# Performance work log

Hardware: AMD Instinct MI355X
Metric: run time of the kernel (lower is better)

## Reference

```python
import jax, jax.numpy as jnp
import numpy as np

WS = 14          # window size
NH = 12          # num heads
C = 768          # hidden dim
HD = C // NH     # head dim = 64
MLP = 3072       # mlp dim
EPS = 1e-6


def _layernorm(x, g, b):
    mu = jnp.mean(x, axis=-1, keepdims=True)
    var = jnp.mean(jnp.square(x - mu), axis=-1, keepdims=True)
    return (x - mu) * jax.lax.rsqrt(var + EPS) * g + b


def setup_inputs() -> dict:
    key = jax.random.key(0)
    ks = jax.random.split(key, 8)
    B, H, W = 8, 64, 64
    f32 = jnp.float32
    d = {}
    d["x"] = jax.random.normal(ks[0], (B, H, W, C), f32)
    d["ln1_g"] = jnp.ones((C,), f32)
    d["ln1_b"] = jnp.zeros((C,), f32)
    d["qkv_w"] = (jax.random.normal(ks[1], (C, 3 * C), f32) * 0.02)
    d["qkv_b"] = jnp.zeros((3 * C,), f32)
    d["proj_w"] = (jax.random.normal(ks[2], (C, C), f32) * 0.02)
    d["proj_b"] = jnp.zeros((C,), f32)
    d["rel_pos_h"] = (jax.random.normal(ks[3], (2 * WS - 1, HD), f32) * 0.02)
    d["rel_pos_w"] = (jax.random.normal(ks[4], (2 * WS - 1, HD), f32) * 0.02)
    d["ln2_g"] = jnp.ones((C,), f32)
    d["ln2_b"] = jnp.zeros((C,), f32)
    d["mlp_w1"] = (jax.random.normal(ks[5], (C, MLP), f32) * 0.02)
    d["mlp_b1"] = jnp.zeros((MLP,), f32)
    d["mlp_w2"] = (jax.random.normal(ks[6], (MLP, C), f32) * 0.02)
    d["mlp_b2"] = jnp.zeros((C,), f32)
    return d


def reference(x, ln1_g, ln1_b, qkv_w, qkv_b, proj_w, proj_b,
              rel_pos_h, rel_pos_w, ln2_g, ln2_b,
              mlp_w1, mlp_b1, mlp_w2, mlp_b2):
    B, H, W, _ = x.shape
    xn = _layernorm(x, ln1_g, ln1_b)

    # ---- window partition (pad to multiple of WS) ----
    pad_h = (-H) % WS
    pad_w = (-W) % WS
    Hp, Wp = H + pad_h, W + pad_w
    xp = jnp.pad(xn, ((0, 0), (0, pad_h), (0, pad_w), (0, 0)))
    # [B, Hp/WS, WS, Wp/WS, WS, C] -> [Bn, WS, WS, C]
    win = xp.reshape(B, Hp // WS, WS, Wp // WS, WS, C)
    win = win.transpose(0, 1, 3, 2, 4, 5).reshape(-1, WS, WS, C)
    Bn = win.shape[0]
    N = WS * WS

    # ---- attention with decomposed relative position bias ----
    qkv = win.reshape(Bn, N, C) @ qkv_w + qkv_b                 # [Bn, N, 3C]
    qkv = qkv.reshape(Bn, N, 3, NH, HD).transpose(2, 0, 3, 1, 4)
    qkv = qkv.reshape(3, Bn * NH, N, HD)
    q, k, v = qkv[0], qkv[1], qkv[2]

    scale = HD ** -0.5
    attn = jnp.einsum('bnd,bmd->bnm', q * scale, k)             # [Bn*NH, N, N]

    # rel coords: q_size == k_size == WS, rel_pos already has 2*WS-1 rows
    coords = jnp.arange(WS)[:, None] - jnp.arange(WS)[None, :] + (WS - 1)
    Rh = rel_pos_h[coords]                                      # [WS, WS, HD]
    Rw = rel_pos_w[coords]                                      # [WS, WS, HD]
    rq = q.reshape(Bn * NH, WS, WS, HD)
    rel_h = jnp.einsum('bhwc,hkc->bhwk', rq, Rh)                # [B', WS, WS, WS]
    rel_w = jnp.einsum('bhwc,wkc->bhwk', rq, Rw)
    attn = (attn.reshape(Bn * NH, WS, WS, WS, WS)
            + rel_h[:, :, :, :, None]
            + rel_w[:, :, :, None, :]).reshape(Bn * NH, N, N)

    attn = jax.nn.softmax(attn, axis=-1)
    out = jnp.einsum('bnm,bmd->bnd', attn, v)                   # [Bn*NH, N, HD]
    out = out.reshape(Bn, NH, WS, WS, HD).transpose(0, 2, 3, 1, 4).reshape(Bn, WS, WS, C)
    out = out @ proj_w + proj_b

    # ---- window unpartition ----
    out = out.reshape(B, Hp // WS, Wp // WS, WS, WS, C)
    out = out.transpose(0, 1, 3, 2, 4, 5).reshape(B, Hp, Wp, C)[:, :H, :W, :]

    x1 = x + out
    y = _layernorm(x1, ln2_g, ln2_b)
    y = jax.nn.gelu(y @ mlp_w1 + mlp_b1, approximate=False) @ mlp_w2 + mlp_b2
    return x1 + y
```

## Files before the change

kernel.cpp:

```cpp
#include <hip/hip_runtime.h>
#include <hip/hip_bf16.h>
#include <cstdint>
#include <cstddef>

using bf16 = __hip_bfloat16;
typedef __attribute__((ext_vector_type(8))) short short8;
typedef __attribute__((ext_vector_type(4))) float f32x4;

typedef __attribute__((address_space(1))) const void as1_void;
typedef __attribute__((address_space(3))) void as3_void;

__device__ __forceinline__ f32x4 mfma16x16x32(short8 a, short8 b, f32x4 c) {
  return __builtin_amdgcn_mfma_f32_16x16x32_bf16(a, b, c, 0, 0, 0);
}

__device__ __forceinline__ void gload_lds16(const void* g, void* l) {
  __builtin_amdgcn_global_load_lds((as1_void*)g, (as3_void*)l, 16, 0, 0);
}

__device__ __forceinline__ uint32_t cvtpk(float a, float b) {
  uint32_t r;
  asm("v_cvt_pk_bf16_f32 %0, %1, %2" : "=v"(r) : "v"(a), "v"(b));
  return r;
}

__device__ __forceinline__ float gelu_f(float v) {
  const float u = 0.7978845608f * v * (1.f + 0.044715f * v * v);
  const float e = __expf(-2.f * fabsf(u));
  const float t = (1.f - e) / (1.f + e);
  return 0.5f * v * (1.f + (u < 0.f ? -t : t));
}

static constexpr int MROWS = 39200;
static constexpr int MPAD  = 39296;
static constexpr int TOK2  = 32768;

__global__ __launch_bounds__(256)
void transpose_cast(const float* __restrict__ in, bf16* __restrict__ out, int K, int N) {
  __shared__ float t[32][33];
  const int tx = threadIdx.x & 31, ty = threadIdx.x >> 5;
  const int bx = blockIdx.x, by = blockIdx.y;
  const int x = bx * 32 + tx;
  for (int r = ty; r < 32; r += 8)
    t[r][tx] = in[(size_t)(by * 32 + r) * N + x];
  __syncthreads();
  const int xo = by * 32 + tx;
  for (int r = ty; r < 32; r += 8)
    out[(size_t)(bx * 32 + r) * K + xo] = __float2bfloat16(t[tx][r]);
}

__global__ __launch_bounds__(256)
void ln1_partition(const float* __restrict__ x, const float* __restrict__ g,
                   const float* __restrict__ bb, bf16* __restrict__ out) {
  const int token = blockIdx.x * 4 + (threadIdx.x >> 6);
  const int lane = threadIdx.x & 63;
  const int win = token / 196, tok = token % 196;
  const int b_ = win / 25, wh = (win / 5) % 5, ww = win % 5;
  const int i = tok / 14, j = tok % 14;
  const int h = wh * 14 + i, w = ww * 14 + j;
  bf16* o = out + (size_t)token * 768;
  if (h >= 64 || w >= 64) {
    for (int t = 0; t < 12; ++t) o[lane + 64 * t] = __float2bfloat16(0.f);
    return;
  }
  const float* src = x + ((size_t)((b_ * 64 + h) * 64 + w)) * 768;
  float vals[12], s = 0.f, ss = 0.f;
  #pragma unroll
  for (int t = 0; t < 12; ++t) {
    float v = src[lane + 64 * t];
    vals[t] = v; s += v; ss += v * v;
  }
  #pragma unroll
  for (int d = 32; d > 0; d >>= 1) { s += __shfl_xor(s, d); ss += __shfl_xor(ss, d); }
  const float mu = s * (1.f / 768.f);
  const float var = ss * (1.f / 768.f) - mu * mu;
  const float inv = rsqrtf(var + 1e-6f);
  #pragma unroll
  for (int t = 0; t < 12; ++t) {
    const int c = lane + 64 * t;
    o[c] = __float2bfloat16((vals[t] - mu) * inv * g[c] + bb[c]);
  }
}

__global__ __launch_bounds__(256)
void ln2_kernel(const float* __restrict__ x1, const float* __restrict__ g,
                const float* __restrict__ bb, bf16* __restrict__ out) {
  const int token = blockIdx.x * 4 + (threadIdx.x >> 6);
  const int lane = threadIdx.x & 63;
  const float* src = x1 + (size_t)token * 768;
  bf16* o = out + (size_t)token * 768;
  float vals[12], s = 0.f, ss = 0.f;
  #pragma unroll
  for (int t = 0; t < 12; ++t) {
    float v = src[lane + 64 * t];
    vals[t] = v; s += v; ss += v * v;
  }
  #pragma unroll
  for (int d = 32; d > 0; d >>= 1) { s += __shfl_xor(s, d); ss += __shfl_xor(ss, d); }
  const float mu = s * (1.f / 768.f);
  const float var = ss * (1.f / 768.f) - mu * mu;
  const float inv = rsqrtf(var + 1e-6f);
  #pragma unroll
  for (int t = 0; t < 12; ++t) {
    const int c = lane + 64 * t;
    o[c] = __float2bfloat16((vals[t] - mu) * inv * g[c] + bb[c]);
  }
}

template<int EPI>
__global__ __launch_bounds__(256)
void gemm_bf16(const bf16* __restrict__ A, const bf16* __restrict__ Bt,
               const float* __restrict__ bias, int K, int Mreal,
               const float* __restrict__ fin, float* __restrict__ fout,
               bf16* __restrict__ ob0, bf16* __restrict__ ob1, bf16* __restrict__ ob2) {
  __shared__ __align__(16) bf16 SMEM[16384];
  bf16* const lA0 = SMEM;
  bf16* const lA1 = SMEM + 4096;
  bf16* const lB0 = SMEM + 8192;
  bf16* const lB1 = SMEM + 12288;
  const int tid = threadIdx.x;
  const int lane = tid & 63, wv = tid >> 6;
  const int lr = lane & 15, hi = lane >> 4;
  const int wm = wv >> 1, wn = wv & 1;

  const int gx = gridDim.x;
  const int nwg = gx * gridDim.y;
  int lin = blockIdx.y * gx + blockIdx.x;
  {
    const int q8 = nwg >> 3, r8 = nwg & 7;
    const int xcd = lin & 7, pos = lin >> 3;
    lin = (xcd < r8 ? xcd * (q8 + 1) : r8 * (q8 + 1) + (xcd - r8) * q8) + pos;
  }
  const size_t arow0 = (size_t)(lin / gx) * 128;
  const size_t brow0 = (size_t)(lin % gx) * 128;
  f32x4 acc[4][4] = {};

  auto stage = [&](bf16* bufA, bf16* bufB, int kt) {
    const int k0 = kt * 32;
    #pragma unroll
    for (int it = 0; it < 2; ++it) {
      const int seg = it * 256 + tid;
      const int row = seg >> 2, kq = seg & 3;
      const size_t dst = (size_t)(it * 256 + wv * 64) * 8;
      if constexpr (EPI == 1) {
        const int k = k0 + kq * 8;
        gload_lds16(A + ((size_t)(k >> 6) * MPAD + arow0 + row) * 64 + (k & 63), bufA + dst);
      } else {
        gload_lds16(A + (arow0 + row) * K + k0 + kq * 8, bufA + dst);
      }
      gload_lds16(Bt + (brow0 + row) * K + k0 + kq * 8, bufB + dst);
    }
  };
  auto compute = [&](const bf16* bufA, const bf16* bufB) {
    short8 af[4], bfr[4];
    #pragma unroll
    for (int m = 0; m < 4; ++m) af[m] = *(const short8*)&bufA[(wm * 64 + m * 16 + lr) * 32 + hi * 8];
    #pragma unroll
    for (int n = 0; n < 4; ++n) bfr[n] = *(const short8*)&bufB[(wn * 64 + n * 16 + lr) * 32 + hi * 8];
    #pragma unroll
    for (int m = 0; m < 4; ++m)
      #pragma unroll
      for (int n = 0; n < 4; ++n)
        acc[m][n] = mfma16x16x32(af[m], bfr[n], acc[m][n]);
  };

  const int nt = K >> 5;
  stage(lA0, lB0, 0);
  __syncthreads();
  for (int t = 0; t < nt; t += 2) {
    if (t + 1 < nt) stage(lA1, lB1, t + 1);
    compute(lA0, lB0);
    __syncthreads();
    if (t + 2 < nt) stage(lA0, lB0, t + 2);
    compute(lA1, lB1);
    __syncthreads();
  }

  if constexpr (EPI == 0) {
    bf16* ct = SMEM;
    #pragma unroll
    for (int n = 0; n < 4; ++n) {
      const int col = wn * 64 + n * 16 + lr;
      const float bv = bias[(int)brow0 + col];
      #pragma unroll
      for (int m = 0; m < 4; ++m) {
        #pragma unroll
        for (int e = 0; e < 4; ++e) {
          const int row = wm * 64 + m * 16 + hi * 4 + e;
          const float v = acc[m][n][e] + bv;
          const int byte = (row << 8) + (col << 1);
          *(bf16*)((char*)ct + (byte ^ ((row & 7) << 5))) = __float2bfloat16(v);
        }
      }
    }
    __syncthreads();
    #pragma unroll
    for (int i = 0; i < 8; ++i) {
      const int lin16 = i * 256 + tid;
      const int row = lin16 >> 4;
      const int u   = lin16 & 15;
      const int byte = (row << 8) + (u << 4);
      const short8 val = *(const short8*)((char*)ct + (byte ^ ((row & 7) << 5)));
      const int grow = (int)arow0 + row;
      const int gcol = (int)brow0 + u * 8;
      if (grow < Mreal) {
        const int which = gcol / 768, head = (gcol >> 6) % 12, d = gcol & 63;
        bf16* dstb = (which == 0) ? ob0 : ((which == 1) ? ob1 : ob2);
        *(short8*)&dstb[((size_t)head * MPAD + grow) * 64 + d] = val;
      }
    }
  } else {
    #pragma unroll
    for (int n = 0; n < 4; ++n) {
      const int col = (int)brow0 + wn * 64 + n * 16 + lr;
      const float bv = bias[col];
      #pragma unroll
      for (int m = 0; m < 4; ++m) {
        #pragma unroll
        for (int e = 0; e < 4; ++e) {
          const int row = (int)arow0 + wm * 64 + m * 16 + hi * 4 + e;
          const float v = acc[m][n][e] + bv;
          if (row < Mreal) {
            const int win = row / 196, tok = row % 196;
            const int b_ = win / 25, wh = (win / 5) % 5, ww = win % 5;
            const int i = tok / 14, j = tok % 14;
            const int h = wh * 14 + i, w = ww * 14 + j;
            if (h < 64 && w < 64) {
              const size_t idx = ((size_t)((b_ * 64 + h) * 64 + w)) * 768 + col;
              fout[idx] = fin[idx] + v;
            }
          }
        }
      }
    }
  }
}

template<int EPI>
__global__ __launch_bounds__(512)
void gemm256(const bf16* __restrict__ A, const bf16* __restrict__ Bt,
             const float* __restrict__ bias, int K,
             const float* __restrict__ fin, float* __restrict__ fout,
             bf16* __restrict__ ob0) {
  __shared__ __align__(16) char SMEM[65536];
  char* const bA0 = SMEM;
  char* const bB0 = SMEM + 16384;
  char* const bA1 = SMEM + 32768;
  char* const bB1 = SMEM + 49152;
  const int tid = threadIdx.x;
  const int lane = tid & 63, wv = tid >> 6;
  const int lr = lane & 15, hi = lane >> 4;
  const int wm = wv >> 2, wn = wv & 3;

  const int gx = gridDim.x;
  const int nwg = gx * gridDim.y;
  int lin = blockIdx.y * gx + blockIdx.x;
  {
    const int q8 = nwg >> 3, r8 = nwg & 7;
    const int xcd = lin & 7, pos = lin >> 3;
    lin = (xcd < r8 ? xcd * (q8 + 1) : r8 * (q8 + 1) + (xcd - r8) * q8) + pos;
  }
  const size_t arow0 = (size_t)(lin / gx) * 256;
  const size_t brow0 = (size_t)(lin % gx) * 256;

  f32x4 acc[8][4] = {};

  auto stage = [&](int kt, char* dA, char* dB) {
    const int k0 = kt * 32;
    #pragma unroll
    for (int j = 0; j < 2; ++j) {
      const int unit = j * 512 + tid;
      const int r = unit >> 2, s = unit & 3;
      const int kk = ((s ^ (r & 3)) << 3);
      gload_lds16(A + (arow0 + r) * (size_t)K + k0 + kk, dA + unit * 16);
      gload_lds16(Bt + (brow0 + r) * (size_t)K + k0 + kk, dB + unit * 16);
    }
  };
  auto compute = [&](const char* sA, const char* sB) {
    short8 bfr[4];
    #pragma unroll
    for (int n = 0; n < 4; ++n) {
      const int br = wn * 64 + n * 16 + lr;
      bfr[n] = *(const short8*)(sB + br * 64 + ((hi ^ (br & 3)) << 4));
    }
    #pragma unroll
    for (int m = 0; m < 8; ++m) {
      const int ar = wm * 128 + m * 16 + lr;
      const short8 af = *(const short8*)(sA + ar * 64 + ((hi ^ (ar & 3)) << 4));
      #pragma unroll
      for (int n = 0; n < 4; ++n)
        acc[m][n] = mfma16x16x32(af, bfr[n], acc[m][n]);
    }
  };

  const int nt = K >> 5;
  stage(0, bA0, bB0);
  stage(1, bA1, bB1);
  for (int t = 0; t < nt; t += 2) {
    asm volatile("s_waitcnt vmcnt(4)" ::: "memory");
    __builtin_amdgcn_s_barrier();
    __builtin_amdgcn_s_setprio(1);
    compute(bA0, bB0);
    __builtin_amdgcn_s_setprio(0);
    asm volatile("s_waitcnt lgkmcnt(0)" ::: "memory");
    __builtin_amdgcn_s_barrier();
    if (t + 2 < nt) { stage(t + 2, bA0, bB0);
                      asm volatile("s_waitcnt vmcnt(4)" ::: "memory"); }
    else            { asm volatile("s_waitcnt vmcnt(0)" ::: "memory"); }
    __builtin_amdgcn_s_barrier();
    __builtin_amdgcn_s_setprio(1);
    compute(bA1, bB1);
    __builtin_amdgcn_s_setprio(0);
    asm volatile("s_waitcnt lgkmcnt(0)" ::: "memory");
    __builtin_amdgcn_s_barrier();
    if (t + 3 < nt) stage(t + 3, bA1, bB1);
  }

  if constexpr (EPI == 2) {
    char* ep = SMEM + wv * 8192;
    #pragma unroll
    for (int h = 0; h < 2; ++h) {
      #pragma unroll
      for (int m2 = 0; m2 < 4; ++m2) {
        #pragma unroll
        for (int n = 0; n < 4; ++n) {
          const int col = n * 16 + lr;
          const float bv = bias[(int)brow0 + wn * 64 + col];
          #pragma unroll
          for (int e = 0; e < 4; ++e) {
            const int row_l = m2 * 16 + hi * 4 + e;
            const float v = gelu_f(acc[h * 4 + m2][n][e] + bv);
            *(bf16*)(ep + row_l * 128 + (((col >> 3) ^ (row_l & 7)) << 4) + ((col & 7) << 1))
                = __float2bfloat16(v);
          }
        }
      }
      #pragma unroll
      for (int p = 0; p < 8; ++p) {
        const int row_l = p * 8 + (lane >> 3);
        const int slot  = lane & 7;
        const short8 val = *(const short8*)(ep + row_l * 128 + ((slot ^ (row_l & 7)) << 4));
        const size_t grow = arow0 + wm * 128 + h * 64 + row_l;
        const int gcol = (int)brow0 + wn * 64 + slot * 8;
        *(short8*)&ob0[grow * 3072 + gcol] = val;
      }
    }
  } else {
    #pragma unroll
    for (int n = 0; n < 4; ++n) {
      const int col = (int)brow0 + wn * 64 + n * 16 + lr;
      const float bv = bias[col];
      #pragma unroll
      for (int m = 0; m < 8; ++m) {
        #pragma unroll
        for (int e = 0; e < 4; ++e) {
          const size_t row = arow0 + wm * 128 + m * 16 + hi * 4 + e;
          const size_t idx = row * 768 + col;
          fout[idx] = fin[idx] + acc[m][n][e] + bv;
        }
      }
    }
  }
}

__global__ __launch_bounds__(512, 2)
void attn_kernel(const bf16* __restrict__ qb, const bf16* __restrict__ kb,
                 const bf16* __restrict__ vb, const float* __restrict__ rph,
                 const float* __restrict__ rpw, bf16* __restrict__ aout) {
  __shared__ __align__(16) char SM[65248];
  bf16* pbh    = (bf16*)SM;
  bf16* pbw    = (bf16*)(SM + 4096);
  bf16* Gh     = (bf16*)(SM + 8192);
  bf16* Gw     = (bf16*)(SM + 23168);
  char* klds   = SM;
  char* vtb    = SM + 25600;
  bf16* relh_s = (bf16*)(SM + 54272);
  bf16* relw_s = (bf16*)(SM + 59760);

  const int bh = blockIdx.x;
  const int win = bh / 12, head = bh % 12;
  const size_t base = ((size_t)head * MPAD + win * 196) * 64;
  const bf16* Q  = qb + base;
  const bf16* Kp = kb + base;
  const bf16* Vp = vb + base;
  const int tid = threadIdx.x, lane = tid & 63, wv = tid >> 6;
  const int lr = lane & 15, hi = lane >> 4;

  for (int i = tid; i < 32 * 64; i += 512) {
    const int r = i >> 6, c = i & 63;
    const bool ok = r < 27;
    pbh[i] = __float2bfloat16(ok ? rph[r * 64 + c] : 0.f);
    pbw[i] = __float2bfloat16(ok ? rpw[r * 64 + c] : 0.f);
  }
  __syncthreads();
  {
    short8 bh00 = *(const short8*)&pbh[(lr) * 64 + hi * 8];
    short8 bh01 = *(const short8*)&pbh[(lr) * 64 + 32 + hi * 8];
    short8 bh10 = *(const short8*)&pbh[(16 + lr) * 64 + hi * 8];
    short8 bh11 = *(const short8*)&pbh[(16 + lr) * 64 + 32 + hi * 8];
    short8 bw00 = *(const short8*)&pbw[(lr) * 64 + hi * 8];
    short8 bw01 = *(const short8*)&pbw[(lr) * 64 + 32 + hi * 8];
    short8 bw10 = *(const short8*)&pbw[(16 + lr) * 64 + hi * 8];
    short8 bw11 = *(const short8*)&pbw[(16 + lr) * 64 + 32 + hi * 8];
    for (int mt = wv; mt < 13; mt += 8) {
      const short8 a0 = *(const short8*)&Q[(mt * 16 + lr) * 64 + hi * 8];
      const short8 a1 = *(const short8*)&Q[(mt * 16 + lr) * 64 + 32 + hi * 8];
      f32x4 g0 = {}, g1 = {}, g2 = {}, g3 = {};
      g0 = mfma16x16x32(a0, bh00, g0); g0 = mfma16x16x32(a1, bh01, g0);
      g1 = mfma16x16x32(a0, bh10, g1); g1 = mfma16x16x32(a1, bh11, g1);
      g2 = mfma16x16x32(a0, bw00, g2); g2 = mfma16x16x32(a1, bw01, g2);
      g3 = mfma16x16x32(a0, bw10, g3); g3 = mfma16x16x32(a1, bw11, g3);
      #pragma unroll
      for (int e = 0; e < 4; ++e) {
        const int row = mt * 16 + hi * 4 + e;
        Gh[row * 36 + lr]      = __float2bfloat16(g0[e]);
        Gh[row * 36 + 16 + lr] = __float2bfloat16(g1[e]);
        Gw[row * 36 + lr]      = __float2bfloat16(g2[e]);
        Gw[row * 36 + 16 + lr] = __float2bfloat16(g3[e]);
      }
    }
  }
  __syncthreads();
  bf16 ghr[6], gwr[6];
  #pragma unroll
  for (int t = 0; t < 6; ++t) {
    const int i = tid + t * 512;
    if (i < 196 * 14) {
      const int q = i / 14, kk = i - (i / 14) * 14;
      const int rh = q / 14 - kk + 13;
      const int rw2 = q - (q / 14) * 14 - kk + 13;
      ghr[t] = Gh[q * 36 + rh];
      gwr[t] = Gw[q * 36 + rw2];
    }
  }
  __syncthreads();
  #pragma unroll
  for (int t = 0; t < 6; ++t) {
    const int i = tid + t * 512;
    if (i < 196 * 14) { relh_s[i] = ghr[t]; relw_s[i] = gwr[t]; }
  }
  for (int c = wv; c < 25; c += 8) {
    const int row = c * 8 + (lane >> 3);
    const int ch  = (lane & 7) ^ (row & 7);
    gload_lds16(Kp + row * 64 + ch * 8, klds + c * 1024);
  }
  for (int i = tid; i < 196 * 8; i += 512) {
    const int key = i >> 3, dg = (i & 7) * 8;
    const short8 v = *(const short8*)&Vp[key * 64 + dg];
    #pragma unroll
    for (int j = 0; j < 8; ++j) {
      const int idx = (dg + j) * 448 + key * 2;
      *(bf16*)(vtb + (idx ^ (j << 4))) = ((const bf16*)&v)[j];
    }
  }
  for (int i = tid; i < 64 * 28; i += 512) {
    const int d = i / 28, key = 196 + i - (i / 28) * 28;
    const int idx = d * 448 + key * 2;
    *(bf16*)(vtb + (idx ^ ((d & 7) << 4))) = __float2bfloat16(0.f);
  }
  __syncthreads();

  for (int qt = wv; qt < 13; qt += 8) {
    const int q = qt * 16 + lr;
    const int qc = q < 196 ? q : 195;
    const short8 bq0 = *(const short8*)&Q[(qt * 16 + lr) * 64 + hi * 8];
    const short8 bq1 = *(const short8*)&Q[(qt * 16 + lr) * 64 + 32 + hi * 8];
    f32x4 s[13];
    __builtin_amdgcn_s_setprio(1);
    #pragma unroll
    for (int nt = 0; nt < 13; ++nt) {
      const int key = nt * 16 + lr;
      const char* kr = klds + key * 128;
      const short8 ka0 = *(const short8*)(kr + (((hi) ^ (key & 7)) << 4));
      const short8 ka1 = *(const short8*)(kr + (((hi + 4) ^ (key & 7)) << 4));
      f32x4 z = {};
      z = mfma16x16x32(ka0, bq0, z);
      z = mfma16x16x32(ka1, bq1, z);
      s[nt] = z;
    }
    __builtin_amdgcn_s_setprio(0);
    float mx = -3.0e38f;
    #pragma unroll
    for (int nt = 0; nt < 13; ++nt) {
      #pragma unroll
      for (int e = 0; e < 4; ++e) {
        const int key = nt * 16 + hi * 4 + e;
        const int kh = key / 14, kw = key - kh * 14;
        float v = s[nt][e] * 0.125f + __bfloat162float(relh_s[qc * 14 + kh])
                                    + __bfloat162float(relw_s[qc * 14 + kw]);
        v = (key < 196) ? v : -3.0e38f;
        s[nt][e] = v;
        mx = fmaxf(mx, v);
      }
    }
    mx = fmaxf(mx, __shfl_xor(mx, 16));
    mx = fmaxf(mx, __shfl_xor(mx, 32));
    float sm = 0.f;
    uint32_t pk0[14], pk1[14];
    #pragma unroll
    for (int nt = 0; nt < 13; ++nt) {
      const float p0 = __expf(s[nt][0] - mx);
      const float p1 = __expf(s[nt][1] - mx);
      const float p2 = __expf(s[nt][2] - mx);
      const float p3 = __expf(s[nt][3] - mx);
      sm += (p0 + p1) + (p2 + p3);
      pk0[nt] = cvtpk(p0, p1);
      pk1[nt] = cvtpk(p2, p3);
    }
    pk0[13] = 0u; pk1[13] = 0u;
    sm += __shfl_xor(sm, 16);
    sm += __shfl_xor(sm, 32);
    const float rinv = 1.f / sm;
    f32x4 o[4] = {};
    #pragma unroll
    for (int kk = 0; kk < 7; ++kk) {
      const uint32_t x0 = pk0[2 * kk],     x1 = pk1[2 * kk];
      const uint32_t y0 = pk0[2 * kk + 1], y1 = pk1[2 * kk + 1];
      const uint32_t s0 = (hi < 2) ? y0 : x0, s1 = (hi < 2) ? y1 : x1;
      const uint32_t t0 = __shfl_xor(s0, 32), t1 = __shfl_xor(s1, 32);
      const uint32_t o0 = (hi < 2) ? x0 : y0, o1 = (hi < 2) ? x1 : y1;
      const bool sendOwn = (hi == 1) || (hi == 2);
      const uint32_t u0 = sendOwn ? o0 : t0, u1 = sendOwn ? o1 : t1;
      const uint32_t r0 = __shfl_xor(u0, 16), r1 = __shfl_xor(u1, 16);
      union { uint32_t u[4]; short8 v; } pf;
      pf.u[0] = (hi == 0) ? x0 : ((hi == 2) ? t0 : r0);
      pf.u[1] = (hi == 0) ? x1 : ((hi == 2) ? t1 : r1);
      pf.u[2] = (hi == 3) ? y0 : ((hi == 1) ? t0 : r0);
      pf.u[3] = (hi == 3) ? y1 : ((hi == 1) ? t1 : r1);
      __builtin_amdgcn_s_setprio(1);
      #pragma unroll
      for (int n2 = 0; n2 < 4; ++n2) {
        const int d = n2 * 16 + lr;
        const int idx = d * 448 + (kk * 32 + hi * 8) * 2;
        const short8 va = *(const short8*)(vtb + (idx ^ ((lr & 7) << 4)));
        o[n2] = mfma16x16x32(va, pf.v, o[n2]);
      }
      __builtin_amdgcn_s_setprio(0);
    }
    if (q < 196) {
      bf16* orow = aout + ((size_t)head * MPAD + win * 196 + q) * 64;
      #pragma unroll
      for (int n2 = 0; n2 < 4; ++n2) {
        uint32_t d0 = cvtpk(o[n2][0] * rinv, o[n2][1] * rinv);
        uint32_t d1 = cvtpk(o[n2][2] * rinv, o[n2][3] * rinv);
        uint32_t* dst = (uint32_t*)&orow[n2 * 16 + hi * 4];
        dst[0] = d0; dst[1] = d1;
      }
    }
  }
}

extern "C" void kernel_launch(void* const* d_in, const int* in_sizes, int n_in,
                              void* d_out, int out_size, void* d_ws, size_t ws_size,
                              hipStream_t stream) {
  (void)in_sizes; (void)n_in; (void)out_size; (void)ws_size;
  const float* x      = (const float*)d_in[0];
  const float* ln1_g  = (const float*)d_in[1];
  const float* ln1_b  = (const float*)d_in[2];
  const float* qkv_w  = (const float*)d_in[3];
  const float* qkv_b  = (const float*)d_in[4];
  const float* proj_w = (const float*)d_in[5];
  const float* proj_b = (const float*)d_in[6];
  const float* rph    = (const float*)d_in[7];
  const float* rpw    = (const float*)d_in[8];
  const float* ln2_g  = (const float*)d_in[9];
  const float* ln2_b  = (const float*)d_in[10];
  const float* w1     = (const float*)d_in[11];
  const float* b1v    = (const float*)d_in[12];
  const float* w2     = (const float*)d_in[13];
  const float* b2v    = (const float*)d_in[14];
  float* outp = (float*)d_out;

  char* ws = (char*)d_ws;
  size_t off = 0;
  auto alloc = [&](size_t bytes) { char* p = ws + off; off += (bytes + 255) & ~(size_t)255; return p; };
  bf16* qkv_wt  = (bf16*)alloc((size_t)2304 * 768 * 2);
  bf16* proj_wt = (bf16*)alloc((size_t)768 * 768 * 2);
  bf16* w1t     = (bf16*)alloc((size_t)3072 * 768 * 2);
  bf16* w2t     = (bf16*)alloc((size_t)768 * 3072 * 2);
  const size_t szB1 = (size_t)MPAD * 768 * 2;
  const size_t szB2 = (size_t)TOK2 * 768 * 2;
  char* regB = alloc(szB1 > szB2 ? szB1 : szB2);
  const size_t szQKV = (size_t)3 * 12 * MPAD * 64 * 2;
  const size_t szH   = (size_t)TOK2 * 3072 * 2;
  char* regC = alloc(szQKV > szH ? szQKV : szH);

  bf16* xnwin   = (bf16*)regB;
  bf16* attnout = (bf16*)regB;
  bf16* xn2     = (bf16*)regB;
  bf16* qbuf    = (bf16*)regC;
  bf16* kbuf    = qbuf + (size_t)12 * MPAD * 64;
  bf16* vbuf    = kbuf + (size_t)12 * MPAD * 64;
  bf16* hbuf    = (bf16*)regC;

  transpose_cast<<<dim3(2304 / 32, 768 / 32), 256, 0, stream>>>(qkv_w, qkv_wt, 768, 2304);
  transpose_cast<<<dim3(768 / 32, 768 / 32), 256, 0, stream>>>(proj_w, proj_wt, 768, 768);
  transpose_cast<<<dim3(3072 / 32, 768 / 32), 256, 0, stream>>>(w1, w1t, 768, 3072);
  transpose_cast<<<dim3(768 / 32, 3072 / 32), 256, 0, stream>>>(w2, w2t, 3072, 768);

  ln1_partition<<<dim3(MROWS / 4), 256, 0, stream>>>(x, ln1_g, ln1_b, xnwin);

  gemm_bf16<0><<<dim3(2304 / 128, MPAD / 128), 256, 0, stream>>>(
      xnwin, qkv_wt, qkv_b, 768, MROWS, nullptr, nullptr, qbuf, kbuf, vbuf);

  attn_kernel<<<dim3(2400), 512, 0, stream>>>(qbuf, kbuf, vbuf, rph, rpw, attnout);

  gemm_bf16<1><<<dim3(768 / 128, MPAD / 128), 256, 0, stream>>>(
      attnout, proj_wt, proj_b, 768, MROWS, x, outp, nullptr, nullptr, nullptr);

  ln2_kernel<<<dim3(TOK2 / 4), 256, 0, stream>>>(outp, ln2_g, ln2_b, xn2);

  gemm256<2><<<dim3(3072 / 256, TOK2 / 256), 512, 0, stream>>>(
      xn2, w1t, b1v, 768, nullptr, nullptr, hbuf);
  gemm256<3><<<dim3(768 / 256, TOK2 / 256), 512, 0, stream>>>(
      hbuf, w2t, b2v, 3072, outp, outp, nullptr);
}
```

Measured before the change: 1.113 ms.

## Restructure 256x256 GEMM main loop with BK=64 tiles and staggered A/B prefetch

Doubles the K-tile from 32 to 64, which doubles the LDS footprint to 128 KiB, and switches to a new XOR swizzle over 8 16-byte slots. The loop is rewritten as an explicitly unrolled tile routine. A and B loads for future tiles are issued at different points inside the MFMA sequence, so global-to-LDS traffic overlaps compute and there are fewer barriers per K step. The risks are the higher LDS use, which allows only one workgroup per CU, more register pressure, and a subtle wait-count and buffer-reuse protocol that is easy to get wrong.

```diff
diff --git a/kernel.cpp b/kernel.cpp
--- a/kernel.cpp
+++ b/kernel.cpp
@@ -242,11 +242,11 @@
              const float* __restrict__ bias, int K,
              const float* __restrict__ fin, float* __restrict__ fout,
              bf16* __restrict__ ob0) {
-  __shared__ __align__(16) char SMEM[65536];
-  char* const bA0 = SMEM;
-  char* const bB0 = SMEM + 16384;
-  char* const bA1 = SMEM + 32768;
-  char* const bB1 = SMEM + 49152;
+  __shared__ __align__(16) char SMEM[131072];
+  char* const A0 = SMEM;
+  char* const B0 = SMEM + 32768;
+  char* const A1 = SMEM + 65536;
+  char* const B1 = SMEM + 98304;
   const int tid = threadIdx.x;
   const int lane = tid & 63, wv = tid >> 6;
   const int lr = lane & 15, hi = lane >> 4;
@@ -264,59 +264,94 @@
   const size_t brow0 = (size_t)(lin % gx) * 256;
 
   f32x4 acc[8][4] = {};
-
-  auto stage = [&](int kt, char* dA, char* dB) {
-    const int k0 = kt * 32;
-    #pragma unroll
-    for (int j = 0; j < 2; ++j) {
-      const int unit = j * 512 + tid;
-      const int r = unit >> 2, s = unit & 3;
-      const int kk = ((s ^ (r & 3)) << 3);
-      gload_lds16(A + (arow0 + r) * (size_t)K + k0 + kk, dA + unit * 16);
-      gload_lds16(Bt + (brow0 + r) * (size_t)K + k0 + kk, dB + unit * 16);
+  const int nt = K >> 6;
+
+  auto stageOp = [&](int kt, char* dst, const bf16* src, size_t row0) {
+    const int k0 = kt << 6;
+    const int rr = tid >> 3, sd = tid & 7;
+    #pragma unroll
+    for (int s = 0; s < 4; ++s) {
+      const int r = s * 64 + rr;
+      const int q = sd ^ ((r >> 1) & 7);
+      gload_lds16(src + (row0 + r) * (size_t)K + k0 + q * 8, dst + s * 8192 + (tid << 4));
     }
   };
-  auto compute = [&](const char* sA, const char* sB) {
-    short8 bfr[4];
-    #pragma unroll
-    for (int n = 0; n < 4; ++n) {
-      const int br = wn * 64 + n * 16 + lr;
-      bfr[n] = *(const short8*)(sB + br * 64 + ((hi ^ (br & 3)) << 4));
-    }
-    #pragma unroll
-    for (int m = 0; m < 8; ++m) {
-      const int ar = wm * 128 + m * 16 + lr;
-      const short8 af = *(const short8*)(sA + ar * 64 + ((hi ^ (ar & 3)) << 4));
-      #pragma unroll
-      for (int n = 0; n < 4; ++n)
-        acc[m][n] = mfma16x16x32(af, bfr[n], acc[m][n]);
-    }
+  auto rdA = [&](const char* buf, int mt, int kk) -> short8 {
+    const int r = wm * 128 + mt * 16 + lr;
+    const int slot = (kk * 4 + hi) ^ ((r >> 1) & 7);
+    return *(const short8*)(buf + r * 128 + (slot << 4));
   };
-
-  const int nt = K >> 5;
-  stage(0, bA0, bB0);
-  stage(1, bA1, bB1);
+  auto rdB = [&](const char* buf, int n, int kk) -> short8 {
+    const int r = wn * 64 + n * 16 + lr;
+    const int slot = (kk * 4 + hi) ^ ((r >> 1) & 7);
+    return *(const short8*)(buf + r * 128 + (slot << 4));
+  };
+
+  auto tile = [&](int t, char* cA, char* cB, char* oA) {
+    if (t + 1 >= nt) asm volatile("s_waitcnt vmcnt(0)" ::: "memory");
+    else             asm volatile("s_waitcnt vmcnt(4)" ::: "memory");
+    __builtin_amdgcn_s_barrier();
+    if (t + 1 < nt) stageOp(t + 1, oA, A, arow0);
+    short8 a0 = rdA(cA, 0, 0), a1 = rdA(cA, 1, 0), a2 = rdA(cA, 2, 0), a3 = rdA(cA, 3, 0);
+    short8 b0 = rdB(cB, 0, 0), b1 = rdB(cB, 1, 0), b2 = rdB(cB, 2, 0), b3 = rdB(cB, 3, 0);
+    __builtin_amdgcn_s_setprio(1);
+    acc[0][0] = mfma16x16x32(a0, b0, acc[0][0]); acc[0][1] = mfma16x16x32(a0, b1, acc[0][1]);
+    acc[0][2] = mfma16x16x32(a0, b2, acc[0][2]); acc[0][3] = mfma16x16x32(a0, b3, acc[0][3]);
+    acc[1][0] = mfma16x16x32(a1, b0, acc[1][0]); acc[1][1] = mfma16x16x32(a1, b1, acc[1][1]);
+    acc[1][2] = mfma16x16x32(a1, b2, acc[1][2]); acc[1][3] = mfma16x16x32(a1, b3, acc[1][3]);
+    acc[2][0] = mfma16x16x32(a2, b0, acc[2][0]); acc[2][1] = mfma16x16x32(a2, b1, acc[2][1]);
+    acc[2][2] = mfma16x16x32(a2, b2, acc[2][2]); acc[2][3] = mfma16x16x32(a2, b3, acc[2][3]);
+    acc[3][0] = mfma16x16x32(a3, b0, acc[3][0]); acc[3][1] = mfma16x16x32(a3, b1, acc[3][1]);
+    acc[3][2] = mfma16x16x32(a3, b2, acc[3][2]); acc[3][3] = mfma16x16x32(a3, b3, acc[3][3]);
+    __builtin_amdgcn_s_setprio(0);
+    short8 a4 = rdA(cA, 4, 0), a5 = rdA(cA, 5, 0), a6 = rdA(cA, 6, 0), a7 = rdA(cA, 7, 0);
+    __builtin_amdgcn_s_setprio(1);
+    acc[4][0] = mfma16x16x32(a4, b0, acc[4][0]); acc[4][1] = mfma16x16x32(a4, b1, acc[4][1]);
+    acc[4][2] = mfma16x16x32(a4, b2, acc[4][2]); acc[4][3] = mfma16x16x32(a4, b3, acc[4][3]);
+    acc[5][0] = mfma16x16x32(a5, b0, acc[5][0]); acc[5][1] = mfma16x16x32(a5, b1, acc[5][1]);
+    acc[5][2] = mfma16x16x32(a5, b2, acc[5][2]); acc[5][3] = mfma16x16x32(a5, b3, acc[5][3]);
+    acc[6][0] = mfma16x16x32(a6, b0, acc[6][0]); acc[6][1] = mfma16x16x32(a6, b1, acc[6][1]);
+    acc[6][2] = mfma16x16x32(a6, b2, acc[6][2]); acc[6][3] = mfma16x16x32(a6, b3, acc[6][3]);
+    acc[7][0] = mfma16x16x32(a7, b0, acc[7][0]); acc[7][1] = mfma16x16x32(a7, b1, acc[7][1]);
+    acc[7][2] = mfma16x16x32(a7, b2, acc[7][2]); acc[7][3] = mfma16x16x32(a7, b3, acc[7][3]);
+    __builtin_amdgcn_s_setprio(0);
+    a0 = rdA(cA, 0, 1); a1 = rdA(cA, 1, 1); a2 = rdA(cA, 2, 1); a3 = rdA(cA, 3, 1);
+    b0 = rdB(cB, 0, 1); b1 = rdB(cB, 1, 1); b2 = rdB(cB, 2, 1); b3 = rdB(cB, 3, 1);
+    __builtin_amdgcn_s_setprio(1);
+    acc[0][0] = mfma16x16x32(a0, b0, acc[0][0]); acc[0][1] = mfma16x16x32(a0, b1, acc[0][1]);
+    acc[0][2] = mfma16x16x32(a0, b2, acc[0][2]); acc[0][3] = mfma16x16x32(a0, b3, acc[0][3]);
+    acc[1][0] = mfma16x16x32(a1, b0, acc[1][0]); acc[1][1] = mfma16x16x32(a1, b1, acc[1][1]);
+    acc[1][2] = mfma16x16x32(a1, b2, acc[1][2]); acc[1][3] = mfma16x16x32(a1, b3, acc[1][3]);
+    acc[2][0] = mfma16x16x32(a2, b0, acc[2][0]); acc[2][1] = mfma16x16x32(a2, b1, acc[2][1]);
+    acc[2][2] = mfma16x16x32(a2, b2, acc[2][2]); acc[2][3] = mfma16x16x32(a2, b3, acc[2][3]);
+    acc[3][0] = mfma16x16x32(a3, b0, acc[3][0]); acc[3][1] = mfma16x16x32(a3, b1, acc[3][1]);
+    acc[3][2] = mfma16x16x32(a3, b2, acc[3][2]); acc[3][3] = mfma16x16x32(a3, b3, acc[3][3]);
+    __builtin_amdgcn_s_setprio(0);
+    __builtin_amdgcn_s_barrier();
+    if (t + 2 < nt) stageOp(t + 2, cB, Bt, brow0);
+    a4 = rdA(cA, 4, 1); a5 = rdA(cA, 5, 1); a6 = rdA(cA, 6, 1); a7 = rdA(cA, 7, 1);
+    __builtin_amdgcn_s_setprio(1);
+    acc[4][0] = mfma16x16x32(a4, b0, acc[4][0]); acc[4][1] = mfma16x16x32(a4, b1, acc[4][1]);
+    acc[4][2] = mfma16x16x32(a4, b2, acc[4][2]); acc[4][3] = mfma16x16x32(a4, b3, acc[4][3]);
+    acc[5][0] = mfma16x16x32(a5, b0, acc[5][0]); acc[5][1] = mfma16x16x32(a5, b1, acc[5][1]);
+    acc[5][2] = mfma16x16x32(a5, b2, acc[5][2]); acc[5][3] = mfma16x16x32(a5, b3, acc[5][3]);
+    acc[6][0] = mfma16x16x32(a6, b0, acc[6][0]); acc[6][1] = mfma16x16x32(a6, b1, acc[6][1]);
+    acc[6][2] = mfma16x16x32(a6, b2, acc[6][2]); acc[6][3] = mfma16x16x32(a6, b3, acc[6][3]);
+    acc[7][0] = mfma16x16x32(a7, b0, acc[7][0]); acc[7][1] = mfma16x16x32(a7, b1, acc[7][1]);
+    acc[7][2] = mfma16x16x32(a7, b2, acc[7][2]); acc[7][3] = mfma16x16x32(a7, b3, acc[7][3]);
+    __builtin_amdgcn_s_setprio(0);
+  };
+
+  stageOp(0, B0, Bt, brow0);
+  stageOp(0, A0, A, arow0);
+  stageOp(1, B1, Bt, brow0);
   for (int t = 0; t < nt; t += 2) {
-    asm volatile("s_waitcnt vmcnt(4)" ::: "memory");
+    tile(t,     A0, B0, A1);
+    tile(t + 1, A1, B1, A0);
+  }
+
+  if constexpr (EPI == 2) {
     __builtin_amdgcn_s_barrier();
-    __builtin_amdgcn_s_setprio(1);
-    compute(bA0, bB0);
-    __builtin_amdgcn_s_setprio(0);
-    asm volatile("s_waitcnt lgkmcnt(0)" ::: "memory");
-    __builtin_amdgcn_s_barrier();
-    if (t + 2 < nt) { stage(t + 2, bA0, bB0);
-                      asm volatile("s_waitcnt vmcnt(4)" ::: "memory"); }
-    else            { asm volatile("s_waitcnt vmcnt(0)" ::: "memory"); }
-    __builtin_amdgcn_s_barrier();
-    __builtin_amdgcn_s_setprio(1);
-    compute(bA1, bB1);
-    __builtin_amdgcn_s_setprio(0);
-    asm volatile("s_waitcnt lgkmcnt(0)" ::: "memory");
-    __builtin_amdgcn_s_barrier();
-    if (t + 3 < nt) stage(t + 3, bA1, bB1);
-  }
-
-  if constexpr (EPI == 2) {
     char* ep = SMEM + wv * 8192;
     #pragma unroll
     for (int h = 0; h < 2; ++h) {
```

Result: no change. 1.121 ms (+0.7%).

## Restructure gemm256 mainloop into 8-phase ping-pong schedule with finer-grained LDS staging

Applied to the files above, without the earlier changes.

Replaces the two-stage K=32 double buffer in the 256x256 GEMM with a 128KB LDS layout. It holds two K=64 tiles, each split into k-halves for A and B, and the main loop becomes eight phases. Each phase reads one half of the A fragments, issues one global-to-LDS load for a future sub-tile, then runs 16 MFMAs under a barrier and raised priority. This interleaves loads with compute at a finer grain to hide memory latency. The swizzle also changes to use (row>>1)&3 to reduce LDS bank conflicts. The 128KB of LDS limits occupancy to one workgroup per CU, and the schedule depends on the vmcnt counting being exactly right.

```diff
diff --git a/kernel.cpp b/kernel.cpp
--- a/kernel.cpp
+++ b/kernel.cpp
@@ -236,17 +236,79 @@
   }
 }
 
+__device__ __forceinline__ short8 rd_frag(const char* reg, int row, int hi) {
+  const int cpos = hi ^ ((row >> 1) & 3);
+  return *(const short8*)(reg + row * 64 + (cpos << 4));
+}
+
+template<int MH, bool READB, int VMN>
+__device__ __forceinline__ void gphase(
+    const char* aR, const char* bR, int wm, int wn, int lr, int hi, int tid,
+    f32x4 (&acc)[8][4], short8& b0, short8& b1, short8& b2, short8& b3,
+    const bf16* ssrc, size_t srow, int K, int skt, int skh, char* sdst, int nt) {
+  const int abase = wm * 128 + MH * 64 + lr;
+  short8 a0 = rd_frag(aR, abase,      hi);
+  short8 a1 = rd_frag(aR, abase + 16, hi);
+  short8 a2 = rd_frag(aR, abase + 32, hi);
+  short8 a3 = rd_frag(aR, abase + 48, hi);
+  if constexpr (READB) {
+    const int bbase = wn * 64 + lr;
+    b0 = rd_frag(bR, bbase,      hi);
+    b1 = rd_frag(bR, bbase + 16, hi);
+    b2 = rd_frag(bR, bbase + 32, hi);
+    b3 = rd_frag(bR, bbase + 48, hi);
+  }
+  if (skt < nt) {
+    const int k0 = (skt << 6) + (skh << 5);
+    #pragma unroll
+    for (int j = 0; j < 2; ++j) {
+      const int d = tid + j * 512;
+      const int r = d >> 2;
+      const int c = (d & 3) ^ ((r >> 1) & 3);
+      gload_lds16(ssrc + (srow + r) * (size_t)K + k0 + c * 8, sdst + d * 16);
+    }
+  }
+  __builtin_amdgcn_s_barrier();
+  asm volatile("s_waitcnt lgkmcnt(0)" ::: "memory");
+  __builtin_amdgcn_sched_barrier(0);
+  __builtin_amdgcn_s_setprio(1);
+  acc[MH*4+0][0] = mfma16x16x32(a0, b0, acc[MH*4+0][0]);
+  acc[MH*4+0][1] = mfma16x16x32(a0, b1, acc[MH*4+0][1]);
+  acc[MH*4+0][2] = mfma16x16x32(a0, b2, acc[MH*4+0][2]);
+  acc[MH*4+0][3] = mfma16x16x32(a0, b3, acc[MH*4+0][3]);
+  acc[MH*4+1][0] = mfma16x16x32(a1, b0, acc[MH*4+1][0]);
+  acc[MH*4+1][1] = mfma16x16x32(a1, b1, acc[MH*4+1][1]);
+  acc[MH*4+1][2] = mfma16x16x32(a1, b2, acc[MH*4+1][2]);
+  acc[MH*4+1][3] = mfma16x16x32(a1, b3, acc[MH*4+1][3]);
+  acc[MH*4+2][0] = mfma16x16x32(a2, b0, acc[MH*4+2][0]);
+  acc[MH*4+2][1] = mfma16x16x32(a2, b1, acc[MH*4+2][1]);
+  acc[MH*4+2][2] = mfma16x16x32(a2, b2, acc[MH*4+2][2]);
+  acc[MH*4+2][3] = mfma16x16x32(a2, b3, acc[MH*4+2][3]);
+  acc[MH*4+3][0] = mfma16x16x32(a3, b0, acc[MH*4+3][0]);
+  acc[MH*4+3][1] = mfma16x16x32(a3, b1, acc[MH*4+3][1]);
+  acc[MH*4+3][2] = mfma16x16x32(a3, b2, acc[MH*4+3][2]);
+  acc[MH*4+3][3] = mfma16x16x32(a3, b3, acc[MH*4+3][3]);
+  __builtin_amdgcn_s_setprio(0);
+  if constexpr (VMN == 6) asm volatile("s_waitcnt vmcnt(6)" ::: "memory");
+  if constexpr (VMN == 0) asm volatile("s_waitcnt vmcnt(0)" ::: "memory");
+  __builtin_amdgcn_s_barrier();
+}
+
 template<int EPI>
 __global__ __launch_bounds__(512)
 void gemm256(const bf16* __restrict__ A, const bf16* __restrict__ Bt,
              const float* __restrict__ bias, int K,
              const float* __restrict__ fin, float* __restrict__ fout,
              bf16* __restrict__ ob0) {
-  __shared__ __align__(16) char SMEM[65536];
-  char* const bA0 = SMEM;
-  char* const bB0 = SMEM + 16384;
-  char* const bA1 = SMEM + 32768;
-  char* const bB1 = SMEM + 49152;
+  __shared__ __align__(16) char SMEM[131072];
+  char* const A0k0 = SMEM;
+  char* const A0k1 = SMEM + 16384;
+  char* const B0k0 = SMEM + 32768;
+  char* const B0k1 = SMEM + 49152;
+  char* const A1k0 = SMEM + 65536;
+  char* const A1k1 = SMEM + 81920;
+  char* const B1k0 = SMEM + 98304;
+  char* const B1k1 = SMEM + 114688;
   const int tid = threadIdx.x;
   const int lane = tid & 63, wv = tid >> 6;
   const int lr = lane & 15, hi = lane >> 4;
@@ -264,56 +326,53 @@
   const size_t brow0 = (size_t)(lin % gx) * 256;
 
   f32x4 acc[8][4] = {};
-
-  auto stage = [&](int kt, char* dA, char* dB) {
-    const int k0 = kt * 32;
+  short8 b0{}, b1{}, b2{}, b3{};
+  const int nt = K >> 6;
+
+  auto stageU = [&](const bf16* src, size_t row0, int kt, int kh, char* dst) {
+    if (kt >= nt) return;
+    const int k0 = (kt << 6) + (kh << 5);
     #pragma unroll
     for (int j = 0; j < 2; ++j) {
-      const int unit = j * 512 + tid;
-      const int r = unit >> 2, s = unit & 3;
-      const int kk = ((s ^ (r & 3)) << 3);
-      gload_lds16(A + (arow0 + r) * (size_t)K + k0 + kk, dA + unit * 16);
-      gload_lds16(Bt + (brow0 + r) * (size_t)K + k0 + kk, dB + unit * 16);
+      const int d = tid + j * 512;
+      const int r = d >> 2;
+      const int c = (d & 3) ^ ((r >> 1) & 3);
+      gload_lds16(src + (row0 + r) * (size_t)K + k0 + c * 8, dst + d * 16);
     }
   };
-  auto compute = [&](const char* sA, const char* sB) {
-    short8 bfr[4];
-    #pragma unroll
-    for (int n = 0; n < 4; ++n) {
-      const int br = wn * 64 + n * 16 + lr;
-      bfr[n] = *(const short8*)(sB + br * 64 + ((hi ^ (br & 3)) << 4));
-    }
-    #pragma unroll
-    for (int m = 0; m < 8; ++m) {
-      const int ar = wm * 128 + m * 16 + lr;
-      const short8 af = *(const short8*)(sA + ar * 64 + ((hi ^ (ar & 3)) << 4));
-      #pragma unroll
-      for (int n = 0; n < 4; ++n)
-        acc[m][n] = mfma16x16x32(af, bfr[n], acc[m][n]);
-    }
-  };
-
-  const int nt = K >> 5;
-  stage(0, bA0, bB0);
-  stage(1, bA1, bB1);
-  for (int t = 0; t < nt; t += 2) {
-    asm volatile("s_waitcnt vmcnt(4)" ::: "memory");
-    __builtin_amdgcn_s_barrier();
-    __builtin_amdgcn_s_setprio(1);
-    compute(bA0, bB0);
-    __builtin_amdgcn_s_setprio(0);
-    asm volatile("s_waitcnt lgkmcnt(0)" ::: "memory");
-    __builtin_amdgcn_s_barrier();
-    if (t + 2 < nt) { stage(t + 2, bA0, bB0);
-                      asm volatile("s_waitcnt vmcnt(4)" ::: "memory"); }
-    else            { asm volatile("s_waitcnt vmcnt(0)" ::: "memory"); }
-    __builtin_amdgcn_s_barrier();
-    __builtin_amdgcn_s_setprio(1);
-    compute(bA1, bB1);
-    __builtin_amdgcn_s_setprio(0);
-    asm volatile("s_waitcnt lgkmcnt(0)" ::: "memory");
-    __builtin_amdgcn_s_barrier();
-    if (t + 3 < nt) stage(t + 3, bA1, bB1);
+
+  stageU(Bt, brow0, 0, 0, B0k0);
+  stageU(A,  arow0, 0, 0, A0k0);
+  stageU(Bt, brow0, 0, 1, B0k1);
+  stageU(A,  arow0, 0, 1, A0k1);
+  stageU(Bt, brow0, 1, 0, B1k0);
+  stageU(A,  arow0, 1, 0, A1k0);
+  stageU(Bt, brow0, 1, 1, B1k1);
+  asm volatile("s_waitcnt vmcnt(6)" ::: "memory");
+  __builtin_amdgcn_s_barrier();
+
+  const int niter = nt >> 1;
+  for (int it = 0; it < niter - 1; ++it) {
+    const int t = it * 2;
+    gphase<0,true ,-1>(A0k0, B0k0, wm,wn,lr,hi,tid, acc, b0,b1,b2,b3, A,  arow0, K, t+1, 1, A1k1, nt);
+    gphase<1,false,-1>(A0k0, B0k0, wm,wn,lr,hi,tid, acc, b0,b1,b2,b3, Bt, brow0, K, t+2, 0, B0k0, nt);
+    gphase<0,true ,-1>(A0k1, B0k1, wm,wn,lr,hi,tid, acc, b0,b1,b2,b3, A,  arow0, K, t+2, 0, A0k0, nt);
+    gphase<1,false, 6>(A0k1, B0k1, wm,wn,lr,hi,tid, acc, b0,b1,b2,b3, Bt, brow0, K, t+2, 1, B0k1, nt);
+    gphase<0,true ,-1>(A1k0, B1k0, wm,wn,lr,hi,tid, acc, b0,b1,b2,b3, A,  arow0, K, t+2, 1, A0k1, nt);
+    gphase<1,false,-1>(A1k0, B1k0, wm,wn,lr,hi,tid, acc, b0,b1,b2,b3, Bt, brow0, K, t+3, 0, B1k0, nt);
+    gphase<0,true ,-1>(A1k1, B1k1, wm,wn,lr,hi,tid, acc, b0,b1,b2,b3, A,  arow0, K, t+3, 0, A1k0, nt);
+    gphase<1,false, 6>(A1k1, B1k1, wm,wn,lr,hi,tid, acc, b0,b1,b2,b3, Bt, brow0, K, t+3, 1, B1k1, nt);
+  }
+  {
+    const int t = nt - 2;
+    gphase<0,true ,-1>(A0k0, B0k0, wm,wn,lr,hi,tid, acc, b0,b1,b2,b3, A,  arow0, K, t+1, 1, A1k1, nt);
+    gphase<1,false,-1>(A0k0, B0k0, wm,wn,lr,hi,tid, acc, b0,b1,b2,b3, Bt, brow0, K, t+2, 0, B0k0, nt);
+    gphase<0,true ,-1>(A0k1, B0k1, wm,wn,lr,hi,tid, acc, b0,b1,b2,b3, A,  arow0, K, t+2, 0, A0k0, nt);
+    gphase<1,false, 0>(A0k1, B0k1, wm,wn,lr,hi,tid, acc, b0,b1,b2,b3, Bt, brow0, K, t+2, 1, B0k1, nt);
+    gphase<0,true ,-1>(A1k0, B1k0, wm,wn,lr,hi,tid, acc, b0,b1,b2,b3, A,  arow0, K, t+2, 1, A0k1, nt);
+    gphase<1,false,-1>(A1k0, B1k0, wm,wn,lr,hi,tid, acc, b0,b1,b2,b3, Bt, brow0, K, t+3, 0, B1k0, nt);
+    gphase<0,true ,-1>(A1k1, B1k1, wm,wn,lr,hi,tid, acc, b0,b1,b2,b3, A,  arow0, K, t+3, 0, A1k0, nt);
+    gphase<1,false, 0>(A1k1, B1k1, wm,wn,lr,hi,tid, acc, b0,b1,b2,b3, Bt, brow0, K, t+3, 1, B1k1, nt);
   }
 
   if constexpr (EPI == 2) {
```

After: 1.064 ms. 4.4% less time.
